# Kernel optimization log

Measured on AMD Instinct MI355X. Metric: run time of the kernel, lower is better.

Reference implementation:

```python
import jax, jax.numpy as jnp
import numpy as np

HIDDEN = 1024
NUM_HEADS = 16
HEAD_DIM = HIDDEN // NUM_HEADS
B, S = 2, 2048


def setup_inputs() -> dict:
    key = jax.random.key(0)
    ks = jax.random.split(key, 7)
    scale = 1.0 / np.sqrt(HIDDEN)
    return {
        "hidden_states": jax.random.normal(ks[0], (B, S, HIDDEN), dtype=jnp.float32),
        "attention_mask": jnp.ones((B, S), dtype=jnp.float32),
        "Wq": jax.random.normal(ks[1], (HIDDEN, HIDDEN), dtype=jnp.float32) * scale,
        "bq": jax.random.normal(ks[2], (HIDDEN,), dtype=jnp.float32) * 0.02,
        "Wk": jax.random.normal(ks[3], (HIDDEN, HIDDEN), dtype=jnp.float32) * scale,
        "bk": jax.random.normal(ks[4], (HIDDEN,), dtype=jnp.float32) * 0.02,
        "Wv": jax.random.normal(ks[5], (HIDDEN, HIDDEN), dtype=jnp.float32) * scale,
        "bv": jax.random.normal(ks[6], (HIDDEN,), dtype=jnp.float32) * 0.02,
    }


def reference(hidden_states, attention_mask, Wq, bq, Wk, bk, Wv, bv):
    # Linear projections (W stored [in, out], equivalent to torch Linear).
    q = hidden_states @ Wq + bq  # [B,S,H]
    k = hidden_states @ Wk + bk
    v = hidden_states @ Wv + bv

    def split_heads(x):  # [B,S,H] -> [B,nh,S,hd]
        return x.reshape(B, S, NUM_HEADS, HEAD_DIM).transpose(0, 2, 1, 3)

    q, k, v = split_heads(q), split_heads(k), split_heads(v)

    scores = jnp.einsum("bhqd,bhkd->bhqk", q, k) / jnp.sqrt(
        jnp.asarray(HEAD_DIM, dtype=q.dtype))
    min_val = jnp.finfo(scores.dtype).min
    ext_mask = (1.0 - attention_mask[:, None, None, :]) * min_val  # [B,1,1,S]
    scores = scores + ext_mask
    probs = jax.nn.softmax(scores, axis=-1)  # eval mode: no dropout
    ctx = jnp.einsum("bhqk,bhkd->bhqd", probs, v)
    ctx = ctx.transpose(0, 2, 1, 3).reshape(B, S, HIDDEN)
    return ctx
```

## Files before the change

### kernel.cpp

```cpp
#include <hip/hip_runtime.h>
#include <hip/hip_bf16.h>
#include <cstddef>
#include <cstdint>

#define HID 1024
#define NHEADS 16
#define HDIM 64
#define BATCH 2
#define SEQ 2048
#define MROWS (BATCH * SEQ)
#define BHT (BATCH * NHEADS)

typedef __attribute__((ext_vector_type(8))) short s8v;
typedef __attribute__((ext_vector_type(4))) float f4v;
typedef __attribute__((ext_vector_type(2))) unsigned int u2v;

__device__ __forceinline__ unsigned int pkbf(float a, float b) {
    __hip_bfloat162 h = __float22bfloat162_rn(float2{a, b});
    union { __hip_bfloat162 v; unsigned int u; } c; c.v = h; return c.u;
}

__device__ __forceinline__ void lds_load16(void* lds, const void* g) {
    __builtin_amdgcn_global_load_lds(
        (const __attribute__((address_space(1))) void*)g,
        (__attribute__((address_space(3))) void*)lds, 16, 0, 0);
}

__global__ __launch_bounds__(256) void conv_fused_kernel(
    const float* __restrict__ hs, const float* __restrict__ mask,
    const float* __restrict__ Wq, const float* __restrict__ Wk,
    const float* __restrict__ Wv,
    unsigned short* __restrict__ Ah, unsigned short* __restrict__ WTh,
    float* __restrict__ lmask)
{
    if (blockIdx.x < 2048) {
        const int idx = (blockIdx.x * 256 + threadIdx.x) * 8;
        float4 v0 = *(const float4*)&hs[idx];
        float4 v1 = *(const float4*)&hs[idx + 4];
        union { unsigned int w[4]; } pk;
        pk.w[0] = pkbf(v0.x, v0.y);
        pk.w[1] = pkbf(v0.z, v0.w);
        pk.w[2] = pkbf(v1.x, v1.y);
        pk.w[3] = pkbf(v1.z, v1.w);
        *(uint4*)&Ah[idx] = *(uint4*)&pk;
    } else if (blockIdx.x < 2816) {
        const int bid = blockIdx.x - 2048;
        const int z = bid >> 8;
        const int rem = bid & 255;
        const float* W = (z == 0) ? Wq : (z == 1) ? Wk : Wv;
        unsigned short* th = WTh + (size_t)z * HID * HID;

        __shared__ float tile[64][65];
        const int t = threadIdx.x;
        const int kb = (rem >> 4) * 64, nb = (rem & 15) * 64;
        const int c4 = (t & 15) * 4;
        const int r0 = t >> 4;

#pragma unroll
        for (int i = 0; i < 4; ++i) {
            int r = r0 + i * 16;
            float4 v = *(const float4*)&W[(size_t)(kb + r) * HID + nb + c4];
            tile[r][c4 + 0] = v.x; tile[r][c4 + 1] = v.y;
            tile[r][c4 + 2] = v.z; tile[r][c4 + 3] = v.w;
        }
        __syncthreads();
#pragma unroll
        for (int i = 0; i < 4; ++i) {
            int n = r0 + i * 16;
            union { unsigned int w[2]; unsigned long long q; } pk;
            pk.w[0] = pkbf(tile[c4 + 0][n], tile[c4 + 1][n]);
            pk.w[1] = pkbf(tile[c4 + 2][n], tile[c4 + 3][n]);
            *(unsigned long long*)&th[(size_t)(nb + n) * HID + kb + c4] = pk.q;
        }
    } else {
        const int idx = (blockIdx.x - 2816) * 256 + threadIdx.x;
        lmask[idx] = (mask[idx] - 1.0f) * 1e30f;
    }
}

#define QSCALE 0.18033688011112042f

__global__ __launch_bounds__(256, 2) void qkv_mfma_kernel(
    const unsigned short* __restrict__ Ah, const unsigned short* __restrict__ WTh,
    const float* __restrict__ bq, const float* __restrict__ bk,
    const float* __restrict__ bv,
    unsigned short* __restrict__ Qg, unsigned short* __restrict__ Khi,
    unsigned short* __restrict__ VTg)
{
    __shared__ unsigned short S[24576];
    unsigned short* AS = S;
    unsigned short* B0 = S + 8192;
    unsigned short* B1 = S + 16384;

    const int z2 = blockIdx.z;
    const int t = threadIdx.x;
    const int wave = t >> 6, lane = t & 63, quad = lane >> 4, l15 = lane & 15;
    const int sw = l15 & 7;
    const int wm = wave >> 1, wn = wave & 1;
    const int rowBase = blockIdx.x * 128;
    const int colBase = blockIdx.y * 128;

    const int srow8 = lane >> 3;
    const int sc    = lane & 7;

    const unsigned short* BhQ = WTh;
    const unsigned short* BhK = WTh + (size_t)HID * HID;
    const unsigned short* BhV = WTh + (size_t)2 * HID * HID;

    size_t goffA[4], goffB[4];
#pragma unroll
    for (int it = 0; it < 4; ++it) {
        const int row = (wave * 4 + it) * 8 + srow8;
        const int gx = (sc ^ (row & 7)) * 8;
        goffA[it] = (size_t)(rowBase + row) * HID + gx;
        goffB[it] = (size_t)(colBase + row) * HID + gx;
    }

    if (z2 == 0) {
        f4v accq[4][4], acck[4][4];
#pragma unroll
        for (int mf = 0; mf < 4; ++mf)
#pragma unroll
            for (int nf = 0; nf < 4; ++nf) {
                accq[mf][nf] = (f4v){0.f, 0.f, 0.f, 0.f};
                acck[mf][nf] = (f4v){0.f, 0.f, 0.f, 0.f};
            }

        for (int kt = 0; kt < HID / 64; ++kt) {
            const int k0 = kt * 64;
            __syncthreads();
#pragma unroll
            for (int it = 0; it < 4; ++it) {
                lds_load16(&AS[(wave * 4 + it) * 512], &Ah[goffA[it] + k0]);
                lds_load16(&B0[(wave * 4 + it) * 512], &BhQ[goffB[it] + k0]);
                lds_load16(&B1[(wave * 4 + it) * 512], &BhK[goffB[it] + k0]);
            }
            __syncthreads();

#pragma unroll
            for (int kk = 0; kk < 2; ++kk) {
                const int csw = ((kk * 4 + quad) ^ sw) * 8;
                s8v af[4], bfq[4], bfk[4];
#pragma unroll
                for (int mf = 0; mf < 4; ++mf)
                    af[mf] = *(const s8v*)&AS[(wm * 64 + mf * 16 + l15) * 64 + csw];
#pragma unroll
                for (int nf = 0; nf < 4; ++nf) {
                    bfq[nf] = *(const s8v*)&B0[(wn * 64 + nf * 16 + l15) * 64 + csw];
                    bfk[nf] = *(const s8v*)&B1[(wn * 64 + nf * 16 + l15) * 64 + csw];
                }
#pragma unroll
                for (int mf = 0; mf < 4; ++mf)
#pragma unroll
                    for (int nf = 0; nf < 4; ++nf) {
                        accq[mf][nf] = __builtin_amdgcn_mfma_f32_16x16x32_bf16(bfq[nf], af[mf], accq[mf][nf], 0, 0, 0);
                        acck[mf][nf] = __builtin_amdgcn_mfma_f32_16x16x32_bf16(bfk[nf], af[mf], acck[mf][nf], 0, 0, 0);
                    }
            }
        }

#pragma unroll
        for (int nf = 0; nf < 4; ++nf) {
            const int n0 = colBase + wn * 64 + nf * 16 + quad * 4;
            const float4 bbq = *(const float4*)&bq[n0];
            const float4 bbk = *(const float4*)&bk[n0];
            const int h = n0 >> 6, d0 = n0 & 63;
#pragma unroll
            for (int mf = 0; mf < 4; ++mf) {
                const int rw = rowBase + wm * 64 + mf * 16 + l15;
                const int b = rw >> 11;
                const int ss = rw & (SEQ - 1);
                const size_t base = ((size_t)(b * NHEADS + h) * SEQ + ss) * HDIM + d0;
                union { unsigned int w[2]; unsigned long long q; } pk;
                pk.w[0] = pkbf((accq[mf][nf][0] + bbq.x) * QSCALE, (accq[mf][nf][1] + bbq.y) * QSCALE);
                pk.w[1] = pkbf((accq[mf][nf][2] + bbq.z) * QSCALE, (accq[mf][nf][3] + bbq.w) * QSCALE);
                *(unsigned long long*)&Qg[base] = pk.q;
                pk.w[0] = pkbf(acck[mf][nf][0] + bbk.x, acck[mf][nf][1] + bbk.y);
                pk.w[1] = pkbf(acck[mf][nf][2] + bbk.z, acck[mf][nf][3] + bbk.w);
                *(unsigned long long*)&Khi[base] = pk.q;
            }
        }
    } else {
        f4v acc[4][4];
#pragma unroll
        for (int mf = 0; mf < 4; ++mf)
#pragma unroll
            for (int nf = 0; nf < 4; ++nf) acc[mf][nf] = (f4v){0.f, 0.f, 0.f, 0.f};

        for (int kt = 0; kt < HID / 64; ++kt) {
            const int k0 = kt * 64;
            __syncthreads();
#pragma unroll
            for (int it = 0; it < 4; ++it) {
                lds_load16(&AS[(wave * 4 + it) * 512], &Ah[goffA[it] + k0]);
                lds_load16(&B0[(wave * 4 + it) * 512], &BhV[goffB[it] + k0]);
            }
            __syncthreads();

#pragma unroll
            for (int kk = 0; kk < 2; ++kk) {
                const int csw = ((kk * 4 + quad) ^ sw) * 8;
                s8v af[4], bf[4];
#pragma unroll
                for (int mf = 0; mf < 4; ++mf)
                    af[mf] = *(const s8v*)&AS[(wm * 64 + mf * 16 + l15) * 64 + csw];
#pragma unroll
                for (int nf = 0; nf < 4; ++nf)
                    bf[nf] = *(const s8v*)&B0[(wn * 64 + nf * 16 + l15) * 64 + csw];
#pragma unroll
                for (int mf = 0; mf < 4; ++mf)
#pragma unroll
                    for (int nf = 0; nf < 4; ++nf)
                        acc[mf][nf] = __builtin_amdgcn_mfma_f32_16x16x32_bf16(af[mf], bf[nf], acc[mf][nf], 0, 0, 0);
            }
        }

#pragma unroll
        for (int nf = 0; nf < 4; ++nf) {
            const int n = colBase + wn * 64 + nf * 16 + l15;
            const float bb = bv[n];
            const int h = n >> 6, d = n & 63;
#pragma unroll
            for (int mf = 0; mf < 4; ++mf) {
                const int rw0 = rowBase + wm * 64 + mf * 16 + quad * 4;
                const int b = rw0 >> 11;
                const int s0 = rw0 & (SEQ - 1);
                union { unsigned int w[2]; unsigned long long q; } pk;
                pk.w[0] = pkbf(acc[mf][nf][0] + bb, acc[mf][nf][1] + bb);
                pk.w[1] = pkbf(acc[mf][nf][2] + bb, acc[mf][nf][3] + bb);
                *(unsigned long long*)&VTg[((size_t)(b * NHEADS + h) * HDIM + d) * SEQ + s0] = pk.q;
            }
        }
    }
}

#define BC 64

__global__ __launch_bounds__(256, 2) void attn_mfma_kernel(
    const unsigned short* __restrict__ Qg, const unsigned short* __restrict__ Khi,
    const unsigned short* __restrict__ VTg,
    const float* __restrict__ lmask, float* __restrict__ out)
{
    __shared__ unsigned short Kb[2][BC * HDIM];
    __shared__ unsigned short Vb[2][BC * HDIM];

    const int t = threadIdx.x;
    const int wave = t >> 6, lane = t & 63, quad = lane >> 4, l15 = lane & 15;
    const int sw = l15 & 7;
    const int bh = blockIdx.x, b = bh >> 4, h = bh & (NHEADS - 1);
    const int qbase = blockIdx.y * 128 + wave * 32;

    const size_t hb = (size_t)bh * SEQ * HDIM;
    const unsigned short* kbase = Khi + hb;
    const unsigned short* vbase = VTg + hb;
    const float* mrow = lmask + b * SEQ;

    s8v qh[2][2];
#pragma unroll
    for (int qf = 0; qf < 2; ++qf)
#pragma unroll
        for (int ds = 0; ds < 2; ++ds) {
            size_t off = hb + (size_t)(qbase + qf * 16 + l15) * HDIM + ds * 32 + quad * 8;
            qh[qf][ds] = *(const s8v*)&Qg[off];
        }

    f4v oacc[2][4];
#pragma unroll
    for (int qf = 0; qf < 2; ++qf)
#pragma unroll
        for (int nf = 0; nf < 4; ++nf) oacc[qf][nf] = (f4v){0.f, 0.f, 0.f, 0.f};
    float l_r[2] = {0.f, 0.f};

    const int srow8 = lane >> 3;
    const int sc    = lane & 7;
    int koff[2], voff[2];
#pragma unroll
    for (int it = 0; it < 2; ++it) {
        const int row = (wave * 2 + it) * 8 + srow8;
        const int gx = (sc ^ (row & 7)) * 8;
        koff[it] = row * HDIM + gx;
        voff[it] = row * SEQ + gx;
    }

#pragma unroll
    for (int it = 0; it < 2; ++it) {
        const int i = wave * 2 + it;
        lds_load16(&Kb[0][i * 512], kbase + koff[it]);
        lds_load16(&Vb[0][i * 512], vbase + voff[it]);
    }
    __syncthreads();

    for (int kt = 0; kt < SEQ / BC; ++kt) {
        const int cur = kt & 1;
        if (kt + 1 < SEQ / BC) {
            const int nxt = cur ^ 1;
#pragma unroll
            for (int it = 0; it < 2; ++it) {
                const int i = wave * 2 + it;
                lds_load16(&Kb[nxt][i * 512], kbase + (kt + 1) * BC * HDIM + koff[it]);
                lds_load16(&Vb[nxt][i * 512], vbase + (kt + 1) * BC + voff[it]);
            }
        }

        float4 msv[4];
#pragma unroll
        for (int mf = 0; mf < 4; ++mf)
            msv[mf] = *(const float4*)&mrow[kt * BC + mf * 16 + quad * 4];

        f4v sacc[2][4];
#pragma unroll
        for (int qf = 0; qf < 2; ++qf)
#pragma unroll
            for (int mf = 0; mf < 4; ++mf)
                sacc[qf][mf] = (f4v){msv[mf].x, msv[mf].y, msv[mf].z, msv[mf].w};

        __builtin_amdgcn_s_setprio(1);
#pragma unroll
        for (int mf = 0; mf < 4; ++mf) {
#pragma unroll
            for (int ds = 0; ds < 2; ++ds) {
                s8v kh = *(const s8v*)&Kb[cur][(mf * 16 + l15) * HDIM + (((ds * 4 + quad) ^ sw) * 8)];
#pragma unroll
                for (int qf = 0; qf < 2; ++qf)
                    sacc[qf][mf] = __builtin_amdgcn_mfma_f32_16x16x32_bf16(kh, qh[qf][ds], sacc[qf][mf], 0, 0, 0);
            }
        }
        __builtin_amdgcn_s_setprio(0);

        s8v pa[2][2];
#pragma unroll
        for (int qf = 0; qf < 2; ++qf) {
            unsigned int wlo[4], whi[4];
            float ps = 0.f;
#pragma unroll
            for (int mf = 0; mf < 4; ++mf) {
                float e0 = __builtin_amdgcn_exp2f(sacc[qf][mf][0]);
                float e1 = __builtin_amdgcn_exp2f(sacc[qf][mf][1]);
                float e2 = __builtin_amdgcn_exp2f(sacc[qf][mf][2]);
                float e3 = __builtin_amdgcn_exp2f(sacc[qf][mf][3]);
                ps += (e0 + e1) + (e2 + e3);
                wlo[mf] = pkbf(e0, e1);
                whi[mf] = pkbf(e2, e3);
            }
            l_r[qf] += ps;
#pragma unroll
            for (int ks = 0; ks < 2; ++ks) {
                unsigned int alo = wlo[ks * 2], blo = wlo[ks * 2 + 1];
                unsigned int ahi = whi[ks * 2], bhi = whi[ks * 2 + 1];
                u2v r;
                r = __builtin_amdgcn_permlane32_swap(alo, blo, false, false); alo = r[0]; blo = r[1];
                r = __builtin_amdgcn_permlane32_swap(ahi, bhi, false, false); ahi = r[0]; bhi = r[1];
                r = __builtin_amdgcn_permlane16_swap(alo, blo, false, false); alo = r[0]; blo = r[1];
                r = __builtin_amdgcn_permlane16_swap(ahi, bhi, false, false); ahi = r[0]; bhi = r[1];
                union { unsigned int w[4]; s8v v; } up;
                up.w[0] = alo; up.w[1] = ahi; up.w[2] = blo; up.w[3] = bhi;
                pa[qf][ks] = up.v;
            }
        }

        __builtin_amdgcn_s_setprio(1);
#pragma unroll
        for (int ks = 0; ks < 2; ++ks) {
            const int csw = ((ks * 4 + quad) ^ sw) * 8;
#pragma unroll
            for (int nf = 0; nf < 4; ++nf) {
                s8v vb = *(const s8v*)&Vb[cur][(nf * 16 + l15) * BC + csw];
                oacc[0][nf] = __builtin_amdgcn_mfma_f32_16x16x32_bf16(pa[0][ks], vb, oacc[0][nf], 0, 0, 0);
                oacc[1][nf] = __builtin_amdgcn_mfma_f32_16x16x32_bf16(pa[1][ks], vb, oacc[1][nf], 0, 0, 0);
            }
        }
        __builtin_amdgcn_s_setprio(0);
        __syncthreads();
    }

#pragma unroll
    for (int qf = 0; qf < 2; ++qf) {
        float v = l_r[qf];
        v += __shfl_xor(v, 16);
        v += __shfl_xor(v, 32);
        float lv[4];
#pragma unroll
        for (int r = 0; r < 4; ++r)
            lv[r] = 1.0f / __shfl(v, quad * 4 + r);
#pragma unroll
        for (int nf = 0; nf < 4; ++nf)
#pragma unroll
            for (int r = 0; r < 4; ++r) {
                int q = qbase + qf * 16 + quad * 4 + r;
                int d = nf * 16 + l15;
                out[((size_t)b * SEQ + q) * HID + h * HDIM + d] = oacc[qf][nf][r] * lv[r];
            }
    }
}

extern "C" void kernel_launch(void* const* d_in, const int* in_sizes, int n_in,
                              void* d_out, int out_size, void* d_ws, size_t ws_size,
                              hipStream_t stream) {
    const float* hs   = (const float*)d_in[0];
    const float* mask = (const float*)d_in[1];
    const float* Wq   = (const float*)d_in[2];
    const float* bq   = (const float*)d_in[3];
    const float* Wk   = (const float*)d_in[4];
    const float* bk   = (const float*)d_in[5];
    const float* Wv   = (const float*)d_in[6];
    const float* bv   = (const float*)d_in[7];
    float* out = (float*)d_out;

    const size_t N = (size_t)MROWS * HID;
    unsigned short* Qg  = (unsigned short*)d_ws;
    unsigned short* Khi = Qg + N;
    unsigned short* VTg = Qg + 2 * N;
    unsigned short* Ah  = Qg + 3 * N;
    unsigned short* WTh = Qg + 4 * N;
    float* lmask = (float*)(WTh + (size_t)3 * HID * HID);

    conv_fused_kernel<<<2048 + 768 + 16, 256, 0, stream>>>(hs, mask, Wq, Wk, Wv, Ah, WTh, lmask);

    dim3 g1(MROWS / 128, HID / 128, 2);
    qkv_mfma_kernel<<<g1, 256, 0, stream>>>(Ah, WTh, bq, bk, bv, Qg, Khi, VTg);

    dim3 g2(BHT, SEQ / 128);
    attn_mfma_kernel<<<g2, 256, 0, stream>>>(Qg, Khi, VTg, lmask, out);
}
```

Baseline: 169.6 us.

## Split attention block into 8 waves of 16 query rows each

```diff
diff --git a/kernel.cpp b/kernel.cpp
--- a/kernel.cpp
+++ b/kernel.cpp
@@ -236,7 +236,7 @@
 
 #define BC 64
 
-__global__ __launch_bounds__(256, 2) void attn_mfma_kernel(
+__global__ __launch_bounds__(512, 4) void attn_mfma_kernel(
     const unsigned short* __restrict__ Qg, const unsigned short* __restrict__ Khi,
     const unsigned short* __restrict__ VTg,
     const float* __restrict__ lmask, float* __restrict__ out)
@@ -248,58 +248,42 @@
     const int wave = t >> 6, lane = t & 63, quad = lane >> 4, l15 = lane & 15;
     const int sw = l15 & 7;
     const int bh = blockIdx.x, b = bh >> 4, h = bh & (NHEADS - 1);
-    const int qbase = blockIdx.y * 128 + wave * 32;
+    const int qbase = blockIdx.y * 128 + wave * 16;
 
     const size_t hb = (size_t)bh * SEQ * HDIM;
     const unsigned short* kbase = Khi + hb;
     const unsigned short* vbase = VTg + hb;
     const float* mrow = lmask + b * SEQ;
 
-    s8v qh[2][2];
-#pragma unroll
-    for (int qf = 0; qf < 2; ++qf)
-#pragma unroll
-        for (int ds = 0; ds < 2; ++ds) {
-            size_t off = hb + (size_t)(qbase + qf * 16 + l15) * HDIM + ds * 32 + quad * 8;
-            qh[qf][ds] = *(const s8v*)&Qg[off];
-        }
-
-    f4v oacc[2][4];
-#pragma unroll
-    for (int qf = 0; qf < 2; ++qf)
-#pragma unroll
-        for (int nf = 0; nf < 4; ++nf) oacc[qf][nf] = (f4v){0.f, 0.f, 0.f, 0.f};
-    float l_r[2] = {0.f, 0.f};
+    s8v qh[2];
+#pragma unroll
+    for (int ds = 0; ds < 2; ++ds) {
+        size_t off = hb + (size_t)(qbase + l15) * HDIM + ds * 32 + quad * 8;
+        qh[ds] = *(const s8v*)&Qg[off];
+    }
+
+    f4v oacc[4];
+#pragma unroll
+    for (int nf = 0; nf < 4; ++nf) oacc[nf] = (f4v){0.f, 0.f, 0.f, 0.f};
+    float l_r = 0.f;
 
     const int srow8 = lane >> 3;
     const int sc    = lane & 7;
-    int koff[2], voff[2];
-#pragma unroll
-    for (int it = 0; it < 2; ++it) {
-        const int row = (wave * 2 + it) * 8 + srow8;
-        const int gx = (sc ^ (row & 7)) * 8;
-        koff[it] = row * HDIM + gx;
-        voff[it] = row * SEQ + gx;
-    }
-
-#pragma unroll
-    for (int it = 0; it < 2; ++it) {
-        const int i = wave * 2 + it;
-        lds_load16(&Kb[0][i * 512], kbase + koff[it]);
-        lds_load16(&Vb[0][i * 512], vbase + voff[it]);
-    }
+    const int row = wave * 8 + srow8;
+    const int gx = (sc ^ (row & 7)) * 8;
+    const int koff = row * HDIM + gx;
+    const int voff = row * SEQ + gx;
+
+    lds_load16(&Kb[0][wave * 512], kbase + koff);
+    lds_load16(&Vb[0][wave * 512], vbase + voff);
     __syncthreads();
 
     for (int kt = 0; kt < SEQ / BC; ++kt) {
         const int cur = kt & 1;
         if (kt + 1 < SEQ / BC) {
             const int nxt = cur ^ 1;
-#pragma unroll
-            for (int it = 0; it < 2; ++it) {
-                const int i = wave * 2 + it;
-                lds_load16(&Kb[nxt][i * 512], kbase + (kt + 1) * BC * HDIM + koff[it]);
-                lds_load16(&Vb[nxt][i * 512], vbase + (kt + 1) * BC + voff[it]);
-            }
+            lds_load16(&Kb[nxt][wave * 512], kbase + (kt + 1) * BC * HDIM + koff);
+            lds_load16(&Vb[nxt][wave * 512], vbase + (kt + 1) * BC + voff);
         }
 
         float4 msv[4];
@@ -307,12 +291,10 @@
         for (int mf = 0; mf < 4; ++mf)
             msv[mf] = *(const float4*)&mrow[kt * BC + mf * 16 + quad * 4];
 
-        f4v sacc[2][4];
-#pragma unroll
-        for (int qf = 0; qf < 2; ++qf)
-#pragma unroll
-            for (int mf = 0; mf < 4; ++mf)
-                sacc[qf][mf] = (f4v){msv[mf].x, msv[mf].y, msv[mf].z, msv[mf].w};
+        f4v sacc[4];
+#pragma unroll
+        for (int mf = 0; mf < 4; ++mf)
+            sacc[mf] = (f4v){msv[mf].x, msv[mf].y, msv[mf].z, msv[mf].w};
 
         __builtin_amdgcn_s_setprio(1);
 #pragma unroll
@@ -320,42 +302,38 @@
 #pragma unroll
             for (int ds = 0; ds < 2; ++ds) {
                 s8v kh = *(const s8v*)&Kb[cur][(mf * 16 + l15) * HDIM + (((ds * 4 + quad) ^ sw) * 8)];
-#pragma unroll
-                for (int qf = 0; qf < 2; ++qf)
-                    sacc[qf][mf] = __builtin_amdgcn_mfma_f32_16x16x32_bf16(kh, qh[qf][ds], sacc[qf][mf], 0, 0, 0);
+                sacc[mf] = __builtin_amdgcn_mfma_f32_16x16x32_bf16(kh, qh[ds], sacc[mf], 0, 0, 0);
             }
         }
         __builtin_amdgcn_s_setprio(0);
 
-        s8v pa[2][2];
-#pragma unroll
-        for (int qf = 0; qf < 2; ++qf) {
-            unsigned int wlo[4], whi[4];
-            float ps = 0.f;
-#pragma unroll
-            for (int mf = 0; mf < 4; ++mf) {
-                float e0 = __builtin_amdgcn_exp2f(sacc[qf][mf][0]);
-                float e1 = __builtin_amdgcn_exp2f(sacc[qf][mf][1]);
-                float e2 = __builtin_amdgcn_exp2f(sacc[qf][mf][2]);
-                float e3 = __builtin_amdgcn_exp2f(sacc[qf][mf][3]);
-                ps += (e0 + e1) + (e2 + e3);
-                wlo[mf] = pkbf(e0, e1);
-                whi[mf] = pkbf(e2, e3);
-            }
-            l_r[qf] += ps;
-#pragma unroll
-            for (int ks = 0; ks < 2; ++ks) {
-                unsigned int alo = wlo[ks * 2], blo = wlo[ks * 2 + 1];
-                unsigned int ahi = whi[ks * 2], bhi = whi[ks * 2 + 1];
-                u2v r;
-                r = __builtin_amdgcn_permlane32_swap(alo, blo, false, false); alo = r[0]; blo = r[1];
-                r = __builtin_amdgcn_permlane32_swap(ahi, bhi, false, false); ahi = r[0]; bhi = r[1];
-                r = __builtin_amdgcn_permlane16_swap(alo, blo, false, false); alo = r[0]; blo = r[1];
-                r = __builtin_amdgcn_permlane16_swap(ahi, bhi, false, false); ahi = r[0]; bhi = r[1];
-                union { unsigned int w[4]; s8v v; } up;
-                up.w[0] = alo; up.w[1] = ahi; up.w[2] = blo; up.w[3] = bhi;
-                pa[qf][ks] = up.v;
-            }
+        unsigned int wlo[4], whi[4];
+        float ps = 0.f;
+#pragma unroll
+        for (int mf = 0; mf < 4; ++mf) {
+            float e0 = __builtin_amdgcn_exp2f(sacc[mf][0]);
+            float e1 = __builtin_amdgcn_exp2f(sacc[mf][1]);
+            float e2 = __builtin_amdgcn_exp2f(sacc[mf][2]);
+            float e3 = __builtin_amdgcn_exp2f(sacc[mf][3]);
+            ps += (e0 + e1) + (e2 + e3);
+            wlo[mf] = pkbf(e0, e1);
+            whi[mf] = pkbf(e2, e3);
+        }
+        l_r += ps;
+
+        s8v pa[2];
+#pragma unroll
+        for (int ks = 0; ks < 2; ++ks) {
+            unsigned int alo = wlo[ks * 2], blo = wlo[ks * 2 + 1];
+            unsigned int ahi = whi[ks * 2], bhi = whi[ks * 2 + 1];
+            u2v r;
+            r = __builtin_amdgcn_permlane32_swap(alo, blo, false, false); alo = r[0]; blo = r[1];
+            r = __builtin_amdgcn_permlane32_swap(ahi, bhi, false, false); ahi = r[0]; bhi = r[1];
+            r = __builtin_amdgcn_permlane16_swap(alo, blo, false, false); alo = r[0]; blo = r[1];
+            r = __builtin_amdgcn_permlane16_swap(ahi, bhi, false, false); ahi = r[0]; bhi = r[1];
+            union { unsigned int w[4]; s8v v; } up;
+            up.w[0] = alo; up.w[1] = ahi; up.w[2] = blo; up.w[3] = bhi;
+            pa[ks] = up.v;
         }
 
         __builtin_amdgcn_s_setprio(1);
@@ -365,17 +343,15 @@
 #pragma unroll
             for (int nf = 0; nf < 4; ++nf) {
                 s8v vb = *(const s8v*)&Vb[cur][(nf * 16 + l15) * BC + csw];
-                oacc[0][nf] = __builtin_amdgcn_mfma_f32_16x16x32_bf16(pa[0][ks], vb, oacc[0][nf], 0, 0, 0);
-                oacc[1][nf] = __builtin_amdgcn_mfma_f32_16x16x32_bf16(pa[1][ks], vb, oacc[1][nf], 0, 0, 0);
+                oacc[nf] = __builtin_amdgcn_mfma_f32_16x16x32_bf16(pa[ks], vb, oacc[nf], 0, 0, 0);
             }
         }
         __builtin_amdgcn_s_setprio(0);
         __syncthreads();
     }
 
-#pragma unroll
-    for (int qf = 0; qf < 2; ++qf) {
-        float v = l_r[qf];
+    {
+        float v = l_r;
         v += __shfl_xor(v, 16);
         v += __shfl_xor(v, 32);
         float lv[4];
@@ -386,9 +362,9 @@
         for (int nf = 0; nf < 4; ++nf)
 #pragma unroll
             for (int r = 0; r < 4; ++r) {
-                int q = qbase + qf * 16 + quad * 4 + r;
+                int q = qbase + quad * 4 + r;
                 int d = nf * 16 + l15;
-                out[((size_t)b * SEQ + q) * HID + h * HDIM + d] = oacc[qf][nf][r] * lv[r];
+                out[((size_t)b * SEQ + q) * HID + h * HDIM + d] = oacc[nf][r] * lv[r];
             }
     }
 }
@@ -420,5 +396,5 @@
     qkv_mfma_kernel<<<g1, 256, 0, stream>>>(Ah, WTh, bq, bk, bv, Qg, Khi, VTg);
 
     dim3 g2(BHT, SEQ / 128);
-    attn_mfma_kernel<<<g2, 256, 0, stream>>>(Qg, Khi, VTg, lmask, out);
-}
+    attn_mfma_kernel<<<g2, 512, 0, stream>>>(Qg, Khi, VTg, lmask, out);
+}
```

After: 165.7 us. -2.3%, faster.

## Split attention KV range across two blocks and merge partials in combine kernel

Applied to the files above, without the earlier changes.

```diff
diff --git a/kernel.cpp b/kernel.cpp
--- a/kernel.cpp
+++ b/kernel.cpp
@@ -235,11 +235,14 @@
 }
 
 #define BC 64
-
-__global__ __launch_bounds__(256, 2) void attn_mfma_kernel(
+#define NSPLIT 2
+#define TPS (SEQ / BC / NSPLIT)
+
+__global__ __launch_bounds__(256, 4) void attn_mfma_kernel(
     const unsigned short* __restrict__ Qg, const unsigned short* __restrict__ Khi,
     const unsigned short* __restrict__ VTg,
-    const float* __restrict__ lmask, float* __restrict__ out)
+    const float* __restrict__ lmask, float* __restrict__ out,
+    float* __restrict__ PoB, float* __restrict__ Pl)
 {
     __shared__ unsigned short Kb[2][BC * HDIM];
     __shared__ unsigned short Vb[2][BC * HDIM];
@@ -248,6 +251,7 @@
     const int wave = t >> 6, lane = t & 63, quad = lane >> 4, l15 = lane & 15;
     const int sw = l15 & 7;
     const int bh = blockIdx.x, b = bh >> 4, h = bh & (NHEADS - 1);
+    const int z = blockIdx.z;
     const int qbase = blockIdx.y * 128 + wave * 32;
 
     const size_t hb = (size_t)bh * SEQ * HDIM;
@@ -264,12 +268,17 @@
             qh[qf][ds] = *(const s8v*)&Qg[off];
         }
 
-    f4v oacc[2][4];
-#pragma unroll
-    for (int qf = 0; qf < 2; ++qf)
+    s8v ones;
+#pragma unroll
+    for (int j = 0; j < 8; ++j) ones[j] = (short)0x3F80;
+
+    f4v oacc[2][4], lacc[2];
+#pragma unroll
+    for (int qf = 0; qf < 2; ++qf) {
 #pragma unroll
         for (int nf = 0; nf < 4; ++nf) oacc[qf][nf] = (f4v){0.f, 0.f, 0.f, 0.f};
-    float l_r[2] = {0.f, 0.f};
+        lacc[qf] = (f4v){0.f, 0.f, 0.f, 0.f};
+    }
 
     const int srow8 = lane >> 3;
     const int sc    = lane & 7;
@@ -282,30 +291,32 @@
         voff[it] = row * SEQ + gx;
     }
 
+    const int gkt0 = z * TPS;
 #pragma unroll
     for (int it = 0; it < 2; ++it) {
         const int i = wave * 2 + it;
-        lds_load16(&Kb[0][i * 512], kbase + koff[it]);
-        lds_load16(&Vb[0][i * 512], vbase + voff[it]);
+        lds_load16(&Kb[0][i * 512], kbase + gkt0 * BC * HDIM + koff[it]);
+        lds_load16(&Vb[0][i * 512], vbase + gkt0 * BC + voff[it]);
     }
     __syncthreads();
 
-    for (int kt = 0; kt < SEQ / BC; ++kt) {
+    for (int kt = 0; kt < TPS; ++kt) {
+        const int gkt = gkt0 + kt;
         const int cur = kt & 1;
-        if (kt + 1 < SEQ / BC) {
+        if (kt + 1 < TPS) {
             const int nxt = cur ^ 1;
 #pragma unroll
             for (int it = 0; it < 2; ++it) {
                 const int i = wave * 2 + it;
-                lds_load16(&Kb[nxt][i * 512], kbase + (kt + 1) * BC * HDIM + koff[it]);
-                lds_load16(&Vb[nxt][i * 512], vbase + (kt + 1) * BC + voff[it]);
+                lds_load16(&Kb[nxt][i * 512], kbase + (gkt + 1) * BC * HDIM + koff[it]);
+                lds_load16(&Vb[nxt][i * 512], vbase + (gkt + 1) * BC + voff[it]);
             }
         }
 
         float4 msv[4];
 #pragma unroll
         for (int mf = 0; mf < 4; ++mf)
-            msv[mf] = *(const float4*)&mrow[kt * BC + mf * 16 + quad * 4];
+            msv[mf] = *(const float4*)&mrow[gkt * BC + mf * 16 + quad * 4];
 
         f4v sacc[2][4];
 #pragma unroll
@@ -331,18 +342,15 @@
 #pragma unroll
         for (int qf = 0; qf < 2; ++qf) {
             unsigned int wlo[4], whi[4];
-            float ps = 0.f;
 #pragma unroll
             for (int mf = 0; mf < 4; ++mf) {
                 float e0 = __builtin_amdgcn_exp2f(sacc[qf][mf][0]);
                 float e1 = __builtin_amdgcn_exp2f(sacc[qf][mf][1]);
                 float e2 = __builtin_amdgcn_exp2f(sacc[qf][mf][2]);
                 float e3 = __builtin_amdgcn_exp2f(sacc[qf][mf][3]);
-                ps += (e0 + e1) + (e2 + e3);
                 wlo[mf] = pkbf(e0, e1);
                 whi[mf] = pkbf(e2, e3);
             }
-            l_r[qf] += ps;
 #pragma unroll
             for (int ks = 0; ks < 2; ++ks) {
                 unsigned int alo = wlo[ks * 2], blo = wlo[ks * 2 + 1];
@@ -368,29 +376,56 @@
                 oacc[0][nf] = __builtin_amdgcn_mfma_f32_16x16x32_bf16(pa[0][ks], vb, oacc[0][nf], 0, 0, 0);
                 oacc[1][nf] = __builtin_amdgcn_mfma_f32_16x16x32_bf16(pa[1][ks], vb, oacc[1][nf], 0, 0, 0);
             }
+            lacc[0] = __builtin_amdgcn_mfma_f32_16x16x32_bf16(pa[0][ks], ones, lacc[0], 0, 0, 0);
+            lacc[1] = __builtin_amdgcn_mfma_f32_16x16x32_bf16(pa[1][ks], ones, lacc[1], 0, 0, 0);
         }
         __builtin_amdgcn_s_setprio(0);
         __syncthreads();
     }
 
+    float* dst = (z == 0) ? out : PoB;
 #pragma unroll
     for (int qf = 0; qf < 2; ++qf) {
-        float v = l_r[qf];
-        v += __shfl_xor(v, 16);
-        v += __shfl_xor(v, 32);
-        float lv[4];
-#pragma unroll
-        for (int r = 0; r < 4; ++r)
-            lv[r] = 1.0f / __shfl(v, quad * 4 + r);
 #pragma unroll
         for (int nf = 0; nf < 4; ++nf)
 #pragma unroll
             for (int r = 0; r < 4; ++r) {
                 int q = qbase + qf * 16 + quad * 4 + r;
                 int d = nf * 16 + l15;
-                out[((size_t)b * SEQ + q) * HID + h * HDIM + d] = oacc[qf][nf][r] * lv[r];
-            }
-    }
+                dst[((size_t)b * SEQ + q) * HID + h * HDIM + d] = oacc[qf][nf][r];
+            }
+        if (l15 == 0) {
+#pragma unroll
+            for (int r = 0; r < 4; ++r) {
+                int q = qbase + qf * 16 + quad * 4 + r;
+                Pl[((size_t)z * BHT + bh) * SEQ + q] = lacc[qf][r];
+            }
+        }
+    }
+}
+
+__global__ __launch_bounds__(256) void combine_kernel(
+    float* __restrict__ out, const float* __restrict__ PoB,
+    const float* __restrict__ Pl)
+{
+    const int i = blockIdx.x * 256 + threadIdx.x;
+    const int tmp = i >> 4;
+    const int h = tmp & (NHEADS - 1);
+    const int bq = tmp >> 4;
+    const int q = bq & (SEQ - 1);
+    const int b = bq >> 11;
+    const int bh = b * NHEADS + h;
+    const float lA = Pl[(size_t)bh * SEQ + q];
+    const float lB = Pl[((size_t)BHT + bh) * SEQ + q];
+    const float rc = 1.0f / (lA + lB);
+    float4 oA = ((const float4*)out)[i];
+    float4 oB = ((const float4*)PoB)[i];
+    float4 o;
+    o.x = (oA.x + oB.x) * rc;
+    o.y = (oA.y + oB.y) * rc;
+    o.z = (oA.z + oB.z) * rc;
+    o.w = (oA.w + oB.w) * rc;
+    ((float4*)out)[i] = o;
 }
 
 extern "C" void kernel_launch(void* const* d_in, const int* in_sizes, int n_in,
@@ -412,13 +447,17 @@
     unsigned short* VTg = Qg + 2 * N;
     unsigned short* Ah  = Qg + 3 * N;
     unsigned short* WTh = Qg + 4 * N;
-    float* lmask = (float*)(WTh + (size_t)3 * HID * HID);
+    float* PoB   = (float*)(Qg + 3 * N);
+    float* lmask = (float*)(Qg + 5 * N);
+    float* Pl    = (float*)(Qg + 5 * N + 8192);
 
     conv_fused_kernel<<<2048 + 768 + 16, 256, 0, stream>>>(hs, mask, Wq, Wk, Wv, Ah, WTh, lmask);
 
     dim3 g1(MROWS / 128, HID / 128, 2);
     qkv_mfma_kernel<<<g1, 256, 0, stream>>>(Ah, WTh, bq, bk, bv, Qg, Khi, VTg);
 
-    dim3 g2(BHT, SEQ / 128);
-    attn_mfma_kernel<<<g2, 256, 0, stream>>>(Qg, Khi, VTg, lmask, out);
-}
+    dim3 g2(BHT, SEQ / 128, NSPLIT);
+    attn_mfma_kernel<<<g2, 256, 0, stream>>>(Qg, Khi, VTg, lmask, out, PoB, Pl);
+
+    combine_kernel<<<(MROWS * HID / 4) / 256, 256, 0, stream>>>(out, PoB, Pl);
+}
```

New measurement: 174.4 us. +2.8%, slower.

## Split QKV GEMM into uniform per-projection tiles with double-buffered LDS; MFMA row sums

Applied to the files above, without the earlier changes.

```diff
diff --git a/kernel.cpp b/kernel.cpp
--- a/kernel.cpp
+++ b/kernel.cpp
@@ -87,26 +87,18 @@
     unsigned short* __restrict__ Qg, unsigned short* __restrict__ Khi,
     unsigned short* __restrict__ VTg)
 {
-    __shared__ unsigned short S[24576];
-    unsigned short* AS = S;
-    unsigned short* B0 = S + 8192;
-    unsigned short* B1 = S + 16384;
-
-    const int z2 = blockIdx.z;
+    __shared__ unsigned short S[32768];
+
     const int t = threadIdx.x;
     const int wave = t >> 6, lane = t & 63, quad = lane >> 4, l15 = lane & 15;
     const int sw = l15 & 7;
     const int wm = wave >> 1, wn = wave & 1;
     const int rowBase = blockIdx.x * 128;
-    const int colBase = blockIdx.y * 128;
+    const int yb = blockIdx.y;
+    const int colBase = yb * 128;
 
     const int srow8 = lane >> 3;
     const int sc    = lane & 7;
-
-    const unsigned short* BhQ = WTh;
-    const unsigned short* BhK = WTh + (size_t)HID * HID;
-    const unsigned short* BhV = WTh + (size_t)2 * HID * HID;
-
     size_t goffA[4], goffB[4];
 #pragma unroll
     for (int it = 0; it < 4; ++it) {
@@ -116,110 +108,101 @@
         goffB[it] = (size_t)(colBase + row) * HID + gx;
     }
 
-    if (z2 == 0) {
-        f4v accq[4][4], acck[4][4];
-#pragma unroll
-        for (int mf = 0; mf < 4; ++mf)
-#pragma unroll
-            for (int nf = 0; nf < 4; ++nf) {
-                accq[mf][nf] = (f4v){0.f, 0.f, 0.f, 0.f};
-                acck[mf][nf] = (f4v){0.f, 0.f, 0.f, 0.f};
-            }
-
-        for (int kt = 0; kt < HID / 64; ++kt) {
-            const int k0 = kt * 64;
-            __syncthreads();
+    f4v acc[4][4];
+#pragma unroll
+    for (int mf = 0; mf < 4; ++mf)
+#pragma unroll
+        for (int nf = 0; nf < 4; ++nf) acc[mf][nf] = (f4v){0.f, 0.f, 0.f, 0.f};
+
+#pragma unroll
+    for (int it = 0; it < 4; ++it) {
+        lds_load16(&S[(wave * 4 + it) * 512], &Ah[goffA[it]]);
+        lds_load16(&S[8192 + (wave * 4 + it) * 512], &WTh[goffB[it]]);
+    }
+    __syncthreads();
+
+    const bool isQK = (yb < 16);
+
+    for (int kt = 0; kt < HID / 64; ++kt) {
+        const int cur = (kt & 1) << 14;
+        const int nxt = cur ^ 16384;
+        if (kt < HID / 64 - 1) {
+            const int k0 = (kt + 1) * 64;
 #pragma unroll
             for (int it = 0; it < 4; ++it) {
-                lds_load16(&AS[(wave * 4 + it) * 512], &Ah[goffA[it] + k0]);
-                lds_load16(&B0[(wave * 4 + it) * 512], &BhQ[goffB[it] + k0]);
-                lds_load16(&B1[(wave * 4 + it) * 512], &BhK[goffB[it] + k0]);
-            }
-            __syncthreads();
-
-#pragma unroll
-            for (int kk = 0; kk < 2; ++kk) {
-                const int csw = ((kk * 4 + quad) ^ sw) * 8;
-                s8v af[4], bfq[4], bfk[4];
+                lds_load16(&S[nxt + (wave * 4 + it) * 512], &Ah[goffA[it] + k0]);
+                lds_load16(&S[nxt + 8192 + (wave * 4 + it) * 512], &WTh[goffB[it] + k0]);
+            }
+        }
+        const unsigned short* AS = &S[cur];
+        const unsigned short* BS = &S[cur + 8192];
+#pragma unroll
+        for (int kk = 0; kk < 2; ++kk) {
+            const int csw = ((kk * 4 + quad) ^ sw) * 8;
+            s8v af[4], bf[4];
+#pragma unroll
+            for (int mf = 0; mf < 4; ++mf)
+                af[mf] = *(const s8v*)&AS[(wm * 64 + mf * 16 + l15) * 64 + csw];
+#pragma unroll
+            for (int nf = 0; nf < 4; ++nf)
+                bf[nf] = *(const s8v*)&BS[(wn * 64 + nf * 16 + l15) * 64 + csw];
+            if (isQK) {
 #pragma unroll
                 for (int mf = 0; mf < 4; ++mf)
-                    af[mf] = *(const s8v*)&AS[(wm * 64 + mf * 16 + l15) * 64 + csw];
-#pragma unroll
-                for (int nf = 0; nf < 4; ++nf) {
-                    bfq[nf] = *(const s8v*)&B0[(wn * 64 + nf * 16 + l15) * 64 + csw];
-                    bfk[nf] = *(const s8v*)&B1[(wn * 64 + nf * 16 + l15) * 64 + csw];
-                }
+#pragma unroll
+                    for (int nf = 0; nf < 4; ++nf)
+                        acc[mf][nf] = __builtin_amdgcn_mfma_f32_16x16x32_bf16(bf[nf], af[mf], acc[mf][nf], 0, 0, 0);
+            } else {
 #pragma unroll
                 for (int mf = 0; mf < 4; ++mf)
 #pragma unroll
-                    for (int nf = 0; nf < 4; ++nf) {
-                        accq[mf][nf] = __builtin_amdgcn_mfma_f32_16x16x32_bf16(bfq[nf], af[mf], accq[mf][nf], 0, 0, 0);
-                        acck[mf][nf] = __builtin_amdgcn_mfma_f32_16x16x32_bf16(bfk[nf], af[mf], acck[mf][nf], 0, 0, 0);
-                    }
-            }
-        }
-
+                    for (int nf = 0; nf < 4; ++nf)
+                        acc[mf][nf] = __builtin_amdgcn_mfma_f32_16x16x32_bf16(af[mf], bf[nf], acc[mf][nf], 0, 0, 0);
+            }
+        }
+        __syncthreads();
+    }
+
+    if (yb < 8) {
 #pragma unroll
         for (int nf = 0; nf < 4; ++nf) {
             const int n0 = colBase + wn * 64 + nf * 16 + quad * 4;
-            const float4 bbq = *(const float4*)&bq[n0];
-            const float4 bbk = *(const float4*)&bk[n0];
+            const float4 bb = *(const float4*)&bq[n0];
             const int h = n0 >> 6, d0 = n0 & 63;
 #pragma unroll
             for (int mf = 0; mf < 4; ++mf) {
                 const int rw = rowBase + wm * 64 + mf * 16 + l15;
                 const int b = rw >> 11;
                 const int ss = rw & (SEQ - 1);
-                const size_t base = ((size_t)(b * NHEADS + h) * SEQ + ss) * HDIM + d0;
                 union { unsigned int w[2]; unsigned long long q; } pk;
-                pk.w[0] = pkbf((accq[mf][nf][0] + bbq.x) * QSCALE, (accq[mf][nf][1] + bbq.y) * QSCALE);
-                pk.w[1] = pkbf((accq[mf][nf][2] + bbq.z) * QSCALE, (accq[mf][nf][3] + bbq.w) * QSCALE);
-                *(unsigned long long*)&Qg[base] = pk.q;
-                pk.w[0] = pkbf(acck[mf][nf][0] + bbk.x, acck[mf][nf][1] + bbk.y);
-                pk.w[1] = pkbf(acck[mf][nf][2] + bbk.z, acck[mf][nf][3] + bbk.w);
-                *(unsigned long long*)&Khi[base] = pk.q;
+                pk.w[0] = pkbf((acc[mf][nf][0] + bb.x) * QSCALE, (acc[mf][nf][1] + bb.y) * QSCALE);
+                pk.w[1] = pkbf((acc[mf][nf][2] + bb.z) * QSCALE, (acc[mf][nf][3] + bb.w) * QSCALE);
+                *(unsigned long long*)&Qg[((size_t)(b * NHEADS + h) * SEQ + ss) * HDIM + d0] = pk.q;
+            }
+        }
+    } else if (yb < 16) {
+#pragma unroll
+        for (int nf = 0; nf < 4; ++nf) {
+            const int nk = colBase - 1024 + wn * 64 + nf * 16 + quad * 4;
+            const float4 bb = *(const float4*)&bk[nk];
+            const int h = nk >> 6, d0 = nk & 63;
+#pragma unroll
+            for (int mf = 0; mf < 4; ++mf) {
+                const int rw = rowBase + wm * 64 + mf * 16 + l15;
+                const int b = rw >> 11;
+                const int ss = rw & (SEQ - 1);
+                union { unsigned int w[2]; unsigned long long q; } pk;
+                pk.w[0] = pkbf(acc[mf][nf][0] + bb.x, acc[mf][nf][1] + bb.y);
+                pk.w[1] = pkbf(acc[mf][nf][2] + bb.z, acc[mf][nf][3] + bb.w);
+                *(unsigned long long*)&Khi[((size_t)(b * NHEADS + h) * SEQ + ss) * HDIM + d0] = pk.q;
             }
         }
     } else {
-        f4v acc[4][4];
-#pragma unroll
-        for (int mf = 0; mf < 4; ++mf)
-#pragma unroll
-            for (int nf = 0; nf < 4; ++nf) acc[mf][nf] = (f4v){0.f, 0.f, 0.f, 0.f};
-
-        for (int kt = 0; kt < HID / 64; ++kt) {
-            const int k0 = kt * 64;
-            __syncthreads();
-#pragma unroll
-            for (int it = 0; it < 4; ++it) {
-                lds_load16(&AS[(wave * 4 + it) * 512], &Ah[goffA[it] + k0]);
-                lds_load16(&B0[(wave * 4 + it) * 512], &BhV[goffB[it] + k0]);
-            }
-            __syncthreads();
-
-#pragma unroll
-            for (int kk = 0; kk < 2; ++kk) {
-                const int csw = ((kk * 4 + quad) ^ sw) * 8;
-                s8v af[4], bf[4];
-#pragma unroll
-                for (int mf = 0; mf < 4; ++mf)
-                    af[mf] = *(const s8v*)&AS[(wm * 64 + mf * 16 + l15) * 64 + csw];
-#pragma unroll
-                for (int nf = 0; nf < 4; ++nf)
-                    bf[nf] = *(const s8v*)&B0[(wn * 64 + nf * 16 + l15) * 64 + csw];
-#pragma unroll
-                for (int mf = 0; mf < 4; ++mf)
-#pragma unroll
-                    for (int nf = 0; nf < 4; ++nf)
-                        acc[mf][nf] = __builtin_amdgcn_mfma_f32_16x16x32_bf16(af[mf], bf[nf], acc[mf][nf], 0, 0, 0);
-            }
-        }
-
 #pragma unroll
         for (int nf = 0; nf < 4; ++nf) {
-            const int n = colBase + wn * 64 + nf * 16 + l15;
-            const float bb = bv[n];
-            const int h = n >> 6, d = n & 63;
+            const int nv = colBase - 2048 + wn * 64 + nf * 16 + l15;
+            const float bb = bv[nv];
+            const int h = nv >> 6, d = nv & 63;
 #pragma unroll
             for (int mf = 0; mf < 4; ++mf) {
                 const int rw0 = rowBase + wm * 64 + mf * 16 + quad * 4;
@@ -235,8 +218,9 @@
 }
 
 #define BC 64
-
-__global__ __launch_bounds__(256, 2) void attn_mfma_kernel(
+#define NT (SEQ / BC)
+
+__global__ __launch_bounds__(256, 4) void attn_mfma_kernel(
     const unsigned short* __restrict__ Qg, const unsigned short* __restrict__ Khi,
     const unsigned short* __restrict__ VTg,
     const float* __restrict__ lmask, float* __restrict__ out)
@@ -264,12 +248,17 @@
             qh[qf][ds] = *(const s8v*)&Qg[off];
         }
 
-    f4v oacc[2][4];
-#pragma unroll
-    for (int qf = 0; qf < 2; ++qf)
+    s8v ones;
+#pragma unroll
+    for (int j = 0; j < 8; ++j) ones[j] = (short)0x3F80;
+
+    f4v oacc[2][4], lacc[2];
+#pragma unroll
+    for (int qf = 0; qf < 2; ++qf) {
 #pragma unroll
         for (int nf = 0; nf < 4; ++nf) oacc[qf][nf] = (f4v){0.f, 0.f, 0.f, 0.f};
-    float l_r[2] = {0.f, 0.f};
+        lacc[qf] = (f4v){0.f, 0.f, 0.f, 0.f};
+    }
 
     const int srow8 = lane >> 3;
     const int sc    = lane & 7;
@@ -290,9 +279,9 @@
     }
     __syncthreads();
 
-    for (int kt = 0; kt < SEQ / BC; ++kt) {
+    for (int kt = 0; kt < NT; ++kt) {
         const int cur = kt & 1;
-        if (kt + 1 < SEQ / BC) {
+        if (kt + 1 < NT) {
             const int nxt = cur ^ 1;
 #pragma unroll
             for (int it = 0; it < 2; ++it) {
@@ -331,18 +320,15 @@
 #pragma unroll
         for (int qf = 0; qf < 2; ++qf) {
             unsigned int wlo[4], whi[4];
-            float ps = 0.f;
 #pragma unroll
             for (int mf = 0; mf < 4; ++mf) {
                 float e0 = __builtin_amdgcn_exp2f(sacc[qf][mf][0]);
                 float e1 = __builtin_amdgcn_exp2f(sacc[qf][mf][1]);
                 float e2 = __builtin_amdgcn_exp2f(sacc[qf][mf][2]);
                 float e3 = __builtin_amdgcn_exp2f(sacc[qf][mf][3]);
-                ps += (e0 + e1) + (e2 + e3);
                 wlo[mf] = pkbf(e0, e1);
                 whi[mf] = pkbf(e2, e3);
             }
-            l_r[qf] += ps;
 #pragma unroll
             for (int ks = 0; ks < 2; ++ks) {
                 unsigned int alo = wlo[ks * 2], blo = wlo[ks * 2 + 1];
@@ -368,6 +354,8 @@
                 oacc[0][nf] = __builtin_amdgcn_mfma_f32_16x16x32_bf16(pa[0][ks], vb, oacc[0][nf], 0, 0, 0);
                 oacc[1][nf] = __builtin_amdgcn_mfma_f32_16x16x32_bf16(pa[1][ks], vb, oacc[1][nf], 0, 0, 0);
             }
+            lacc[0] = __builtin_amdgcn_mfma_f32_16x16x32_bf16(pa[0][ks], ones, lacc[0], 0, 0, 0);
+            lacc[1] = __builtin_amdgcn_mfma_f32_16x16x32_bf16(pa[1][ks], ones, lacc[1], 0, 0, 0);
         }
         __builtin_amdgcn_s_setprio(0);
         __syncthreads();
@@ -375,13 +363,9 @@
 
 #pragma unroll
     for (int qf = 0; qf < 2; ++qf) {
-        float v = l_r[qf];
-        v += __shfl_xor(v, 16);
-        v += __shfl_xor(v, 32);
         float lv[4];
 #pragma unroll
-        for (int r = 0; r < 4; ++r)
-            lv[r] = 1.0f / __shfl(v, quad * 4 + r);
+        for (int r = 0; r < 4; ++r) lv[r] = 1.0f / lacc[qf][r];
 #pragma unroll
         for (int nf = 0; nf < 4; ++nf)
 #pragma unroll
@@ -416,7 +400,7 @@
 
     conv_fused_kernel<<<2048 + 768 + 16, 256, 0, stream>>>(hs, mask, Wq, Wk, Wv, Ah, WTh, lmask);
 
-    dim3 g1(MROWS / 128, HID / 128, 2);
+    dim3 g1(MROWS / 128, 3 * HID / 128);
     qkv_mfma_kernel<<<g1, 256, 0, stream>>>(Ah, WTh, bq, bk, bv, Qg, Khi, VTg);
 
     dim3 g2(BHT, SEQ / 128);
```

Result: faster. 164.1 us (-3.3%).
